# Optimization experiments

Hardware: AMD Instinct MI355X
Metric: run time of the kernel (lower is better)

The kernel has to match this reference:

```python
import jax, jax.numpy as jnp
import numpy as np

B = 131072
H_DIM = 256
DT = 0.05


def setup_inputs() -> dict:
    key = jax.random.key(0)
    ks = jax.random.split(key, 20)
    w = lambda k, shape, fan_in: jax.random.normal(k, shape, jnp.float32) / np.sqrt(fan_in)
    return {
        "q": jax.random.normal(ks[0], (B, 1), jnp.float32),
        "p": jax.random.normal(ks[1], (B, 1), jnp.float32),
        "u": jax.random.normal(ks[2], (B, 1), jnp.float32),
        "Wk1": w(ks[3], (H_DIM, 2), 2), "bk1": w(ks[4], (H_DIM,), 2),
        "Wk2": w(ks[5], (H_DIM, H_DIM), H_DIM), "bk2": w(ks[6], (H_DIM,), H_DIM),
        "Wk3": w(ks[7], (1, H_DIM), H_DIM), "bk3": w(ks[8], (1,), H_DIM),
        "Wp1": w(ks[9], (H_DIM, 1), 1), "bp1": w(ks[10], (H_DIM,), 1),
        "Wp2": w(ks[11], (H_DIM, H_DIM), H_DIM), "bp2": w(ks[12], (H_DIM,), H_DIM),
        "Wp3": w(ks[13], (1, H_DIM), H_DIM), "bp3": w(ks[14], (1,), H_DIM),
        "b_ctrl": jax.random.normal(ks[15], (1, 1), jnp.float32) * 0.01,
    }


def reference(q, p, u, Wk1, bk1, Wk2, bk2, Wk3, bk3, Wp1, bp1, Wp2, bp2, Wp3, bp3, b_ctrl):
    sp = jax.nn.softplus

    def H(z):  # z: (B, 2) -> (B,)
        qz = z[:, :1]
        hk = sp(z @ Wk1.T + bk1)
        hk = sp(hk @ Wk2.T + bk2)
        T = (hk @ Wk3.T + bk3)[:, 0]
        hp = sp(qz @ Wp1.T + bp1)
        hp = sp(hp @ Wp2.T + bp2)
        V = (hp @ Wp3.T + bp3)[:, 0]
        return T + V

    grad_H = jax.grad(lambda z: H(z).sum())
    # M = J - R with R = 0, J fixed symplectic form
    M = jnp.array([[0.0, 1.0], [-1.0, 0.0]], jnp.float32)
    ctrl = jnp.concatenate([jnp.zeros_like(q), u @ b_ctrl.T], axis=-1)  # (B, 2)

    def dyn(q_, p_):
        # torch detaches z before autograd.grad -> stop_gradient matches semantics
        z = jax.lax.stop_gradient(jnp.concatenate([q_, p_], axis=-1))
        dz = grad_H(z) @ M.T + ctrl
        return dz[:, :1], dz[:, 1:]

    dt = DT
    dq1, dp1 = dyn(q, p)
    dq2, dp2 = dyn(q + 0.5 * dt * dq1, p + 0.5 * dt * dp1)
    dq3, dp3 = dyn(q + 0.5 * dt * dq2, p + 0.5 * dt * dp2)
    dq4, dp4 = dyn(q + dt * dq3, p + dt * dp3)
    q_next = q + dt / 6.0 * (dq1 + 2 * dq2 + 2 * dq3 + dq4)
    p_next = p + dt / 6.0 * (dp1 + 2 * dp2 + 2 * dp3 + dp4)
    return (q_next, p_next)
```

## Files before the change

kernel.cpp:

```cpp
#include <hip/hip_runtime.h>
#include <hip/hip_bf16.h>

#define NB   131072
#define TPB  1024
#define SPB  512

typedef __attribute__((ext_vector_type(8))) short short8;
typedef __attribute__((ext_vector_type(4))) float f32x4;

__device__ __forceinline__ unsigned short f2bf(float f) {
    union { float f; unsigned int u; } v; v.f = f;
    unsigned int r = v.u + 0x7fff + ((v.u >> 16) & 1);
    return (unsigned short)(r >> 16);
}

__device__ __forceinline__ unsigned int cvt_pk_bf16(float lo, float hi) {
    unsigned int r;
    asm("v_cvt_pk_bf16_f32 %0, %1, %2" : "=v"(r) : "v"(lo), "v"(hi));
    return r;
}

__device__ __forceinline__ float row_reduce_add(float x) {
    x += __int_as_float(__builtin_amdgcn_update_dpp(0, __float_as_int(x), 0x128, 0xF, 0xF, true));
    x += __int_as_float(__builtin_amdgcn_update_dpp(0, __float_as_int(x), 0x124, 0xF, 0xF, true));
    x += __int_as_float(__builtin_amdgcn_update_dpp(0, __float_as_int(x), 0x122, 0xF, 0xF, true));
    x += __int_as_float(__builtin_amdgcn_update_dpp(0, __float_as_int(x), 0x121, 0xF, 0xF, true));
    return x;
}

__global__ void prep_weights(const float* __restrict__ Wk2, const float* __restrict__ Wp2,
                             unsigned short* __restrict__ out) {
    int idx = blockIdx.x * blockDim.x + threadIdx.x;
    int n = idx >> 8, k = idx & 255;
    unsigned short a = f2bf(Wk2[idx]);
    out[idx] = a;
    out[65536 + k * 256 + n] = a;
    unsigned short b = f2bf(Wp2[idx]);
    out[131072 + idx] = b;
    out[196608 + k * 256 + n] = b;
}

__launch_bounds__(TPB, 4)
__global__ void phgn_main(const float* __restrict__ q_in, const float* __restrict__ p_in,
                          const float* __restrict__ u_in,
                          const float* __restrict__ Wk1, const float* __restrict__ bk1,
                          const float* __restrict__ bk2, const float* __restrict__ wk3,
                          const float* __restrict__ wp1, const float* __restrict__ bp1,
                          const float* __restrict__ bp2, const float* __restrict__ wp3,
                          const float* __restrict__ bctrl,
                          const unsigned short* __restrict__ Wmats,
                          float* __restrict__ out_q, float* __restrict__ out_p) {
    __shared__ unsigned short bufH0[8192], bufH1[8192];
    __shared__ unsigned short bufG0[8192], bufG1[8192];
    __shared__ float2 qps[SPB];
    __shared__ float2 q0p0[SPB];
    __shared__ float2 accs[SPB];
    __shared__ float  ucs[SPB];
    __shared__ float  slot0[1024], slot1[1024];
    __shared__ float  dHacc[SPB * 2];

    const int tid  = threadIdx.x;
    const int lane = tid & 63;
    const int wave = tid >> 6;
    const int g    = lane >> 4;
    const int l15  = lane & 15;
    const int col  = wave * 16 + l15;
    const int wbase = ((col >> 5) << 9) + (((col >> 3) & 3) << 7) + (col & 7);

    if (tid < SPB) {
        const int sg = blockIdx.x * SPB + tid;
        const float q0 = q_in[sg], p0 = p_in[sg];
        q0p0[tid] = make_float2(q0, p0);
        qps[tid]  = make_float2(q0, p0);
        accs[tid] = make_float2(0.f, 0.f);
        ucs[tid]  = u_in[sg] * bctrl[0];
    }
    __syncthreads();

    const float dt = 0.05f;

    #pragma unroll 1
    for (int st = 0; st < 4; ++st) {
        #pragma unroll 1
        for (int path = 0; path < 2; ++path) {
            const unsigned short* Wf = Wmats + path * 131072;
            const unsigned short* Wb = Wf + 65536;
            const float wq = path ? wp1[col] : Wk1[2*col];
            const float wp = path ? 0.f      : Wk1[2*col+1];
            const float b1 = path ? bp1[col] : bk1[col];
            const float w3 = path ? wp3[col] : wk3[col];
            const float b2 = path ? bp2[col] : bk2[col];

            short8 wfr[8], wbr[8];
            #pragma unroll
            for (int ks = 0; ks < 8; ++ks) {
                wfr[ks] = *(const short8*)(Wf + col * 256 + ks * 32 + g * 8);
                wbr[ks] = *(const short8*)(Wb + col * 256 + ks * 32 + g * 8);
            }

            f32x4 ac, bc;
            unsigned int spkA[4], spkB[4];

            auto phA = [&](int pair, unsigned short* HB, unsigned int* spk) {
                const int mb = pair * 32;
                #pragma unroll
                for (int u = 0; u < 2; ++u) {
                    #pragma unroll
                    for (int r = 0; r < 4; r += 2) {
                        const float4 qq = *(const float4*)&qps[mb + u*16 + g*4 + r];
                        const float a0 = fmaf(wq, qq.x, fmaf(wp, qq.y, b1));
                        const float a1 = fmaf(wq, qq.z, fmaf(wp, qq.w, b1));
                        const float e0 = __expf(a0), e1 = __expf(a1);
                        const float d0 = 1.0f + e0, d1 = 1.0f + e1;
                        const float s0 = e0 * __builtin_amdgcn_rcpf(d0);
                        const float s1 = e1 * __builtin_amdgcn_rcpf(d1);
                        const float h0 = __logf(d0), h1 = __logf(d1);
                        spk[u*2 + (r >> 1)] = cvt_pk_bf16(s0, s1);
                        const unsigned int pk = cvt_pk_bf16(h0, h1);
                        HB[u*4096 + wbase + (g*4 + r    ) * 8] = (unsigned short)(pk & 0xffffu);
                        HB[u*4096 + wbase + (g*4 + r + 1) * 8] = (unsigned short)(pk >> 16);
                    }
                }
            };
            auto phB = [&](const unsigned short* HB, int u) {
                ac = (f32x4){0.f, 0.f, 0.f, 0.f};
                #pragma unroll
                for (int ks = 0; ks < 8; ++ks) {
                    const short8 af = *(const short8*)(HB + u*4096 + ks*512 + lane*8);
                    ac = __builtin_amdgcn_mfma_f32_16x16x32_bf16(af, wfr[ks], ac, 0,0,0);
                }
            };
            auto phC = [&](unsigned short* GB, int u) {
                #pragma unroll
                for (int r = 0; r < 4; r += 2) {
                    float gg[2];
                    #pragma unroll
                    for (int v = 0; v < 2; ++v) {
                        const float a  = ac[r+v] + b2;
                        const float e  = __expf(a);
                        gg[v] = w3 * (e * __builtin_amdgcn_rcpf(1.0f + e));
                    }
                    const unsigned int pk = cvt_pk_bf16(gg[0], gg[1]);
                    GB[u*4096 + wbase + (g*4 + r    ) * 8] = (unsigned short)(pk & 0xffffu);
                    GB[u*4096 + wbase + (g*4 + r + 1) * 8] = (unsigned short)(pk >> 16);
                }
            };
            auto phD = [&](const unsigned short* GB, int u) {
                bc = (f32x4){0.f, 0.f, 0.f, 0.f};
                #pragma unroll
                for (int ns = 0; ns < 8; ++ns) {
                    const short8 ag = *(const short8*)(GB + u*4096 + ns*512 + lane*8);
                    bc = __builtin_amdgcn_mfma_f32_16x16x32_bf16(ag, wbr[ns], bc, 0,0,0);
                }
            };
            auto phE = [&](const unsigned int* spk, int u, float* slot) {
                #pragma unroll
                for (int r = 0; r < 4; ++r) {
                    const unsigned int pk = spk[u*2 + (r >> 1)];
                    const float s1 = __uint_as_float((r & 1) ? (pk & 0xffff0000u) : (pk << 16));
                    const float v  = bc[r] * s1;
                    const float sq = row_reduce_add(v * wq);
                    float sp = 0.f;
                    if (path == 0) sp = row_reduce_add(v * wp);
                    if (l15 == 0) {
                        const int base = wave * 64 + (u*16 + g*4 + r) * 2;
                        slot[base] = sq;
                        if (path == 0) slot[base + 1] = sp;
                    }
                }
            };
            auto phF = [&](int pair, const float* slot) {
                if (tid < 64) {
                    const int m2 = tid >> 1, c = tid & 1;
                    if (path == 0 || c == 0) {
                        float s = 0.f;
                        #pragma unroll
                        for (int w = 0; w < 16; ++w) s += slot[w * 64 + tid];
                        const int di = (pair * 32 + m2) * 2 + c;
                        if (path == 0) dHacc[di] = s;
                        else           dHacc[di] += s;
                    }
                }
            };

            phA(0, bufH0, spkA);
            __syncthreads();
            phB(bufH0,0); phC(bufG0,0); phB(bufH0,1); phC(bufG0,1);
            phA(1, bufH1, spkB);
            __syncthreads();

            #pragma unroll 1
            for (int k2 = 0; k2 < 7; ++k2) {
                const int j = 1 + 2*k2;
                phB(bufH1,0); phD(bufG0,0); phC(bufG1,0); phE(spkA, 0, slot0);
                phB(bufH1,1); phD(bufG0,1); phC(bufG1,1); phE(spkA, 1, slot0);
                if (k2) phF(j - 2, slot1);
                phA(j + 1, bufH0, spkA);
                __syncthreads();
                phB(bufH0,0); phD(bufG1,0); phC(bufG0,0); phE(spkB, 0, slot1);
                phB(bufH0,1); phD(bufG1,1); phC(bufG0,1); phE(spkB, 1, slot1);
                phF(j - 1, slot0);
                phA(j + 2, bufH1, spkB);
                __syncthreads();
            }

            phB(bufH1,0); phD(bufG0,0); phC(bufG1,0); phE(spkA, 0, slot0);
            phB(bufH1,1); phD(bufG0,1); phC(bufG1,1); phE(spkA, 1, slot0);
            phF(13, slot1);
            __syncthreads();
            phD(bufG1,0); phE(spkB, 0, slot1);
            phD(bufG1,1); phE(spkB, 1, slot1);
            phF(14, slot0);
            __syncthreads();
            phF(15, slot1);
            __syncthreads();
        }

        if (tid < SPB) {
            const float dq = dHacc[tid * 2 + 1];
            const float dp = -dHacc[tid * 2 + 0] + ucs[tid];
            const float c = (st == 1 || st == 2) ? 2.f : 1.f;
            float2 acc = accs[tid];
            acc.x += c * dq; acc.y += c * dp;
            accs[tid] = acc;
            if (st < 3) {
                const float hh = (st == 2) ? dt : 0.5f * dt;
                const float2 z0 = q0p0[tid];
                qps[tid] = make_float2(z0.x + hh * dq, z0.y + hh * dp);
            }
        }
        __syncthreads();
    }

    if (tid < SPB) {
        const int sg = blockIdx.x * SPB + tid;
        const float2 z0 = q0p0[tid];
        const float2 acc = accs[tid];
        out_q[sg] = z0.x + (dt / 6.f) * acc.x;
        out_p[sg] = z0.y + (dt / 6.f) * acc.y;
    }
}

extern "C" void kernel_launch(void* const* d_in, const int* in_sizes, int n_in,
                              void* d_out, int out_size, void* d_ws, size_t ws_size,
                              hipStream_t stream) {
    const float* q   = (const float*)d_in[0];
    const float* p   = (const float*)d_in[1];
    const float* u   = (const float*)d_in[2];
    const float* Wk1 = (const float*)d_in[3];
    const float* bk1 = (const float*)d_in[4];
    const float* Wk2 = (const float*)d_in[5];
    const float* bk2 = (const float*)d_in[6];
    const float* Wk3 = (const float*)d_in[7];
    const float* Wp1 = (const float*)d_in[9];
    const float* bp1 = (const float*)d_in[10];
    const float* Wp2 = (const float*)d_in[11];
    const float* bp2 = (const float*)d_in[12];
    const float* Wp3 = (const float*)d_in[13];
    const float* bc  = (const float*)d_in[15];

    unsigned short* wbf = (unsigned short*)d_ws;
    prep_weights<<<256, 256, 0, stream>>>(Wk2, Wp2, wbf);

    float* oq = (float*)d_out;
    phgn_main<<<NB / SPB, TPB, 0, stream>>>(q, p, u, Wk1, bk1, bk2, Wk3, Wp1, bp1, bp2, Wp3,
                                            bc, wbf, oq, oq + NB);
}
```

Measured before the change: 496.5 us.

## Replace DPP row reductions with MFMA for first-layer backward projection

The final backward contraction with the first-layer weights (Wk1/Wp1) now runs as a small bf16 MFMA on values shuffled with ds_bpermute, replacing the per-row DPP reduction chains. Softplus derivatives are no longer kept in registers. They are recomputed from the stored hidden activation as 1-exp(-h), which removes the spk arrays and lowers register pressure. Exponentials and logs use raw v_exp/v_log in base 2 with LOG2E folded into the weights and biases. This adds bf16 rounding to the reduction and to the recomputed derivative, and swaps the MFMA operand order in phD to fit the new layout.

```diff
diff --git a/kernel.cpp b/kernel.cpp
--- a/kernel.cpp
+++ b/kernel.cpp
@@ -7,6 +7,7 @@
 
 typedef __attribute__((ext_vector_type(8))) short short8;
 typedef __attribute__((ext_vector_type(4))) float f32x4;
+typedef __attribute__((ext_vector_type(4))) unsigned short ushort4v;
 
 __device__ __forceinline__ unsigned short f2bf(float f) {
     union { float f; unsigned int u; } v; v.f = f;
@@ -19,13 +20,11 @@
     asm("v_cvt_pk_bf16_f32 %0, %1, %2" : "=v"(r) : "v"(lo), "v"(hi));
     return r;
 }
-
-__device__ __forceinline__ float row_reduce_add(float x) {
-    x += __int_as_float(__builtin_amdgcn_update_dpp(0, __float_as_int(x), 0x128, 0xF, 0xF, true));
-    x += __int_as_float(__builtin_amdgcn_update_dpp(0, __float_as_int(x), 0x124, 0xF, 0xF, true));
-    x += __int_as_float(__builtin_amdgcn_update_dpp(0, __float_as_int(x), 0x122, 0xF, 0xF, true));
-    x += __int_as_float(__builtin_amdgcn_update_dpp(0, __float_as_int(x), 0x121, 0xF, 0xF, true));
-    return x;
+__device__ __forceinline__ float fexp2(float x) {
+    float r; asm("v_exp_f32 %0, %1" : "=v"(r) : "v"(x)); return r;
+}
+__device__ __forceinline__ float flog2(float x) {
+    float r; asm("v_log_f32 %0, %1" : "=v"(r) : "v"(x)); return r;
 }
 
 __global__ void prep_weights(const float* __restrict__ Wk2, const float* __restrict__ Wp2,
@@ -66,6 +65,10 @@
     const int l15  = lane & 15;
     const int col  = wave * 16 + l15;
     const int wbase = ((col >> 5) << 9) + (((col >> 3) & 3) << 7) + (col & 7);
+    const int hbE = (wave >> 1) * 512 + ((wave & 1) * 2 + (g >> 1)) * 128
+                  + l15 * 8 + 4 * (g & 1);
+    const int idxLo = ((g << 5) | l15) << 2;
+    const int idxHi = idxLo + 64;
 
     if (tid < SPB) {
         const int sg = blockIdx.x * SPB + tid;
@@ -78,6 +81,7 @@
     __syncthreads();
 
     const float dt = 0.05f;
+    const float LOG2E = 1.44269504f;
 
     #pragma unroll 1
     for (int st = 0; st < 4; ++st) {
@@ -85,11 +89,11 @@
         for (int path = 0; path < 2; ++path) {
             const unsigned short* Wf = Wmats + path * 131072;
             const unsigned short* Wb = Wf + 65536;
-            const float wq = path ? wp1[col] : Wk1[2*col];
-            const float wp = path ? 0.f      : Wk1[2*col+1];
-            const float b1 = path ? bp1[col] : bk1[col];
-            const float w3 = path ? wp3[col] : wk3[col];
-            const float b2 = path ? bp2[col] : bk2[col];
+            const float wq  = (path ? wp1[col] : Wk1[2*col])   * LOG2E;
+            const float wp  = (path ? 0.f      : Wk1[2*col+1]) * LOG2E;
+            const float b1p = (path ? bp1[col] : bk1[col])     * LOG2E;
+            const float w3  =  path ? wp3[col] : wk3[col];
+            const float b2p = (path ? bp2[col] : bk2[col])     * LOG2E;
 
             short8 wfr[8], wbr[8];
             #pragma unroll
@@ -98,24 +102,39 @@
                 wbr[ks] = *(const short8*)(Wb + col * 256 + ks * 32 + g * 8);
             }
 
+            short8 w1f;
+            {
+                union { int iv[4]; short8 sv; } uu;
+                #pragma unroll
+                for (int d = 0; d < 4; ++d) {
+                    float lo = 0.f, hi = 0.f;
+                    if (g < 2 && l15 < 2) {
+                        const int k0 = wave * 16 + g * 8 + 2 * d;
+                        if (path == 0) {
+                            lo = Wk1[2*k0 + l15];
+                            hi = Wk1[2*k0 + 2 + l15];
+                        } else if (l15 == 0) {
+                            lo = wp1[k0]; hi = wp1[k0 + 1];
+                        }
+                    }
+                    uu.iv[d] = cvt_pk_bf16(lo, hi);
+                }
+                w1f = uu.sv;
+            }
+
             f32x4 ac, bc;
-            unsigned int spkA[4], spkB[4];
-
-            auto phA = [&](int pair, unsigned short* HB, unsigned int* spk) {
+
+            auto phA = [&](int pair, unsigned short* HB) {
                 const int mb = pair * 32;
                 #pragma unroll
                 for (int u = 0; u < 2; ++u) {
                     #pragma unroll
                     for (int r = 0; r < 4; r += 2) {
                         const float4 qq = *(const float4*)&qps[mb + u*16 + g*4 + r];
-                        const float a0 = fmaf(wq, qq.x, fmaf(wp, qq.y, b1));
-                        const float a1 = fmaf(wq, qq.z, fmaf(wp, qq.w, b1));
-                        const float e0 = __expf(a0), e1 = __expf(a1);
-                        const float d0 = 1.0f + e0, d1 = 1.0f + e1;
-                        const float s0 = e0 * __builtin_amdgcn_rcpf(d0);
-                        const float s1 = e1 * __builtin_amdgcn_rcpf(d1);
-                        const float h0 = __logf(d0), h1 = __logf(d1);
-                        spk[u*2 + (r >> 1)] = cvt_pk_bf16(s0, s1);
+                        const float a0 = fmaf(wq, qq.x, fmaf(wp, qq.y, b1p));
+                        const float a1 = fmaf(wq, qq.z, fmaf(wp, qq.w, b1p));
+                        const float h0 = flog2(1.0f + fexp2(a0));
+                        const float h1 = flog2(1.0f + fexp2(a1));
                         const unsigned int pk = cvt_pk_bf16(h0, h1);
                         HB[u*4096 + wbase + (g*4 + r    ) * 8] = (unsigned short)(pk & 0xffffu);
                         HB[u*4096 + wbase + (g*4 + r + 1) * 8] = (unsigned short)(pk >> 16);
@@ -136,8 +155,7 @@
                     float gg[2];
                     #pragma unroll
                     for (int v = 0; v < 2; ++v) {
-                        const float a  = ac[r+v] + b2;
-                        const float e  = __expf(a);
+                        const float e = fexp2(ac[r+v] + b2p);
                         gg[v] = w3 * (e * __builtin_amdgcn_rcpf(1.0f + e));
                     }
                     const unsigned int pk = cvt_pk_bf16(gg[0], gg[1]);
@@ -150,23 +168,35 @@
                 #pragma unroll
                 for (int ns = 0; ns < 8; ++ns) {
                     const short8 ag = *(const short8*)(GB + u*4096 + ns*512 + lane*8);
-                    bc = __builtin_amdgcn_mfma_f32_16x16x32_bf16(ag, wbr[ns], bc, 0,0,0);
-                }
-            };
-            auto phE = [&](const unsigned int* spk, int u, float* slot) {
-                #pragma unroll
-                for (int r = 0; r < 4; ++r) {
-                    const unsigned int pk = spk[u*2 + (r >> 1)];
-                    const float s1 = __uint_as_float((r & 1) ? (pk & 0xffff0000u) : (pk << 16));
-                    const float v  = bc[r] * s1;
-                    const float sq = row_reduce_add(v * wq);
-                    float sp = 0.f;
-                    if (path == 0) sp = row_reduce_add(v * wp);
-                    if (l15 == 0) {
-                        const int base = wave * 64 + (u*16 + g*4 + r) * 2;
-                        slot[base] = sq;
-                        if (path == 0) slot[base + 1] = sp;
-                    }
+                    bc = __builtin_amdgcn_mfma_f32_16x16x32_bf16(wbr[ns], ag, bc, 0,0,0);
+                }
+            };
+            auto phE = [&](const unsigned short* HB, int u, float* slot) {
+                const ushort4v hv = *(const ushort4v*)(HB + u*4096 + hbE);
+                float v0, v1, v2, v3;
+                {
+                    const float h0 = __uint_as_float((unsigned)hv[0] << 16);
+                    const float h1 = __uint_as_float((unsigned)hv[1] << 16);
+                    const float h2 = __uint_as_float((unsigned)hv[2] << 16);
+                    const float h3 = __uint_as_float((unsigned)hv[3] << 16);
+                    v0 = bc[0] * (1.0f - fexp2(-h0));
+                    v1 = bc[1] * (1.0f - fexp2(-h1));
+                    v2 = bc[2] * (1.0f - fexp2(-h2));
+                    v3 = bc[3] * (1.0f - fexp2(-h3));
+                }
+                const int pk01 = (int)cvt_pk_bf16(v0, v1);
+                const int pk23 = (int)cvt_pk_bf16(v2, v3);
+                union { int iv[4]; short8 sv; } af;
+                af.iv[0] = __builtin_amdgcn_ds_bpermute(idxLo, pk01);
+                af.iv[1] = __builtin_amdgcn_ds_bpermute(idxLo, pk23);
+                af.iv[2] = __builtin_amdgcn_ds_bpermute(idxHi, pk01);
+                af.iv[3] = __builtin_amdgcn_ds_bpermute(idxHi, pk23);
+                f32x4 dd = (f32x4){0.f, 0.f, 0.f, 0.f};
+                dd = __builtin_amdgcn_mfma_f32_16x16x32_bf16(af.sv, w1f, dd, 0,0,0);
+                if (l15 < 2) {
+                    #pragma unroll
+                    for (int r = 0; r < 4; ++r)
+                        slot[wave*64 + (u*16 + g*4 + r)*2 + l15] = dd[r];
                 }
             };
             auto phF = [&](int pair, const float* slot) {
@@ -183,33 +213,33 @@
                 }
             };
 
-            phA(0, bufH0, spkA);
+            phA(0, bufH0);
             __syncthreads();
             phB(bufH0,0); phC(bufG0,0); phB(bufH0,1); phC(bufG0,1);
-            phA(1, bufH1, spkB);
+            phA(1, bufH1);
             __syncthreads();
 
             #pragma unroll 1
             for (int k2 = 0; k2 < 7; ++k2) {
                 const int j = 1 + 2*k2;
-                phB(bufH1,0); phD(bufG0,0); phC(bufG1,0); phE(spkA, 0, slot0);
-                phB(bufH1,1); phD(bufG0,1); phC(bufG1,1); phE(spkA, 1, slot0);
+                phB(bufH1,0); phD(bufG0,0); phC(bufG1,0); phE(bufH0, 0, slot0);
+                phB(bufH1,1); phD(bufG0,1); phC(bufG1,1); phE(bufH0, 1, slot0);
                 if (k2) phF(j - 2, slot1);
-                phA(j + 1, bufH0, spkA);
+                phA(j + 1, bufH0);
                 __syncthreads();
-                phB(bufH0,0); phD(bufG1,0); phC(bufG0,0); phE(spkB, 0, slot1);
-                phB(bufH0,1); phD(bufG1,1); phC(bufG0,1); phE(spkB, 1, slot1);
+                phB(bufH0,0); phD(bufG1,0); phC(bufG0,0); phE(bufH1, 0, slot1);
+                phB(bufH0,1); phD(bufG1,1); phC(bufG0,1); phE(bufH1, 1, slot1);
                 phF(j - 1, slot0);
-                phA(j + 2, bufH1, spkB);
+                phA(j + 2, bufH1);
                 __syncthreads();
             }
 
-            phB(bufH1,0); phD(bufG0,0); phC(bufG1,0); phE(spkA, 0, slot0);
-            phB(bufH1,1); phD(bufG0,1); phC(bufG1,1); phE(spkA, 1, slot0);
+            phB(bufH1,0); phD(bufG0,0); phC(bufG1,0); phE(bufH0, 0, slot0);
+            phB(bufH1,1); phD(bufG0,1); phC(bufG1,1); phE(bufH0, 1, slot0);
             phF(13, slot1);
             __syncthreads();
-            phD(bufG1,0); phE(spkB, 0, slot1);
-            phD(bufG1,1); phE(spkB, 1, slot1);
+            phD(bufG1,0); phE(bufH1, 0, slot1);
+            phD(bufG1,1); phE(bufH1, 1, slot1);
             phF(14, slot0);
             __syncthreads();
             phF(15, slot1);
```

Measured after the change: 424.0 us. 1.17x faster.
